# Optimization experiments

Hardware: AMD Instinct MI355X
Metric: run time of the kernel (lower is better)

## Reference

```python
import jax, jax.numpy as jnp
import numpy as np

N = 4096        # nodes
E = 4096        # hyperedges (source math forces E == N)
B = 3           # behaviors
D_IN = 64
HID = 32
OUT = 32
L = 2           # num_layers
EPS = 1e-6      # DynamicPruningGNN.epsilon
DEG_P = 0.008   # ~32 incidences per node


def setup_inputs() -> dict:
    key = jax.random.key(0)
    ks = jax.random.split(key, 12)
    sc = lambda f: 1.0 / np.sqrt(f)
    X = jax.random.normal(ks[0], (N, D_IN), jnp.float32)
    # sparse binary incidence matrices, stored dense as the original does (H.toarray())
    H = (jax.random.uniform(ks[1], (B, N, E)) < DEG_P).astype(jnp.float32)
    return {
        "X": X,
        "H": H,
        "W_init": jax.random.normal(ks[2], (D_IN, HID), jnp.float32) * sc(D_IN),
        "b_init": jnp.zeros((HID,), jnp.float32),
        "W_node": jax.random.normal(ks[3], (L, HID, HID), jnp.float32) * sc(HID),
        "b_node": jnp.zeros((L, HID), jnp.float32),
        "Theta": jax.random.normal(ks[4], (B, HID, HID), jnp.float32) * sc(HID),
        "behavior_importance": jnp.ones((B,), jnp.float32),
        "Wp1": jax.random.normal(ks[5], (HID, HID), jnp.float32) * sc(HID),
        "bp1": jnp.zeros((HID,), jnp.float32),
        "Wp2": jax.random.normal(ks[6], (HID, OUT), jnp.float32) * sc(HID),
        "bp2": jnp.zeros((OUT,), jnp.float32),
    }


def reference(X, H, W_init, b_init, W_node, b_node, Theta,
              behavior_importance, Wp1, bp1, Wp2, bp2):
    # degree normalizers, clamped like np.maximum(deg, epsilon)
    dv = 1.0 / jnp.sqrt(jnp.maximum(H.sum(axis=2), EPS))   # [B, N]  Dv^-1/2
    de = 1.0 / jnp.maximum(H.sum(axis=1), EPS)             # [B, E]  De^-1
    w = jax.nn.softmax(behavior_importance)                # behavior weights

    x = jax.nn.relu(X @ W_init + b_init)                   # initial_transform  [N, HID]
    for l in range(L):
        xw = x @ W_node[l] + b_node[l]                     # node layer          [N, HID]
        y = dv[:, :, None] * xw[None, :, :]                # Dv^-1/2 . XW       [B, N, HID]
        z = jnp.einsum('bne,bnh->beh', H, y) * de[:, :, None]   # De^-1 H^T ...  [B, E, HID]
        u = jnp.einsum('bne,beh->bnh', H, z) * dv[:, :, None]   # Dv^-1/2 H ...  [B, N, HID]
        msg = jnp.einsum('bnh,bhk->bnk', u, Theta)         # per-behavior Theta [B, N, HID]
        x = jax.nn.relu(jnp.einsum('b,bnk->nk', w, msg))   # weighted multi-behavior agg
    # node_projection: Linear -> ReLU -> Linear
    node_emb = jax.nn.relu(x @ Wp1 + bp1) @ Wp2 + bp2      # [N, OUT]
    return node_emb
```

## Files before the change

kernel.cpp:

```cpp
#include <hip/hip_runtime.h>

#define NN 4096
#define EE 4096
#define BB 3
#define DIN 64
#define HID 32
#define MAXDEG 64
#define EPSF 1e-6f
#define CCPAD 8

__global__ void build_sparse(const float* __restrict__ H,
                             int* __restrict__ rowcnt,
                             int* __restrict__ colcnt_pad,
                             unsigned short* __restrict__ csr16,
                             unsigned short* __restrict__ csc16) {
    __shared__ int el[MAXDEG];
    __shared__ int scnt;
    const int bn = blockIdx.x;
    const int tid = threadIdx.x;
    if (tid == 0) scnt = 0;
    if (tid < 32) ((unsigned int*)csc16)[bn * 32 + tid] = 0;
    if (tid < CCPAD) colcnt_pad[bn * CCPAD + tid] = 0;
    __syncthreads();
    const float4* row = (const float4*)(H + (size_t)bn * EE);
    for (int k = tid; k < EE / 4; k += 256) {
        float4 v = row[k];
        int m = (v.x != 0.f) + (v.y != 0.f) + (v.z != 0.f) + (v.w != 0.f);
        if (m) {
            int base = atomicAdd(&scnt, m);
            const int e0 = k * 4;
            if (v.x != 0.f) { if (base < MAXDEG) el[base] = e0;     base++; }
            if (v.y != 0.f) { if (base < MAXDEG) el[base] = e0 + 1; base++; }
            if (v.z != 0.f) { if (base < MAXDEG) el[base] = e0 + 2; base++; }
            if (v.w != 0.f) { if (base < MAXDEG) el[base] = e0 + 3; base++; }
        }
    }
    __syncthreads();
    const int cnt = scnt;
    if (tid == 0) rowcnt[bn] = cnt;
    const int m = min(cnt, MAXDEG);
    if (tid < MAXDEG)
        csr16[(size_t)bn * MAXDEG + tid] = (tid < m) ? (unsigned short)el[tid] : 0;
}

__global__ __launch_bounds__(256) void k_prep(
        const int* __restrict__ rowcnt, const unsigned short* __restrict__ csr16,
        int* __restrict__ colcnt_pad, unsigned short* __restrict__ csc16,
        const float* __restrict__ X,
        const float* __restrict__ Wi, const float* __restrict__ bi,
        const float* __restrict__ Wn0, const float* __restrict__ bn0,
        float* __restrict__ ybuf) {
    __shared__ float sWi[DIN * HID];
    __shared__ float sWn[HID * HID];
    __shared__ float sb0[HID], sb1[HID];
    __shared__ float su[8][HID];
    const int tid = threadIdx.x, lane = tid & 31, g = tid >> 5;
    if (blockIdx.x < NN / 8) {
        for (int i = tid; i < DIN * HID; i += 256) sWi[i] = Wi[i];
        for (int i = tid; i < HID * HID; i += 256) sWn[i] = Wn0[i];
        if (tid < HID) { sb0[tid] = bi[tid]; sb1[tid] = bn0[tid]; }
        __syncthreads();
        const int n = blockIdx.x * 8 + g;
        const float* xr = X + (size_t)n * DIN;
        float acc = sb0[lane];
#pragma unroll 8
        for (int d = 0; d < DIN; d++) acc = fmaf(xr[d], sWi[d * HID + lane], acc);
        su[g][lane] = fmaxf(acc, 0.f);
        float a = sb1[lane];
#pragma unroll
        for (int hh = 0; hh < HID; hh++) a = fmaf(su[g][hh], sWn[hh * HID + lane], a);
#pragma unroll
        for (int b = 0; b < BB; b++) {
            const float c = (float)rowcnt[(b << 12) + n];
            ybuf[((size_t)(b << 12) + n) * HID + lane] = a * rsqrtf(fmaxf(c, EPSF));
        }
    }
    const int r = blockIdx.x * 8 + g;
    const int b = r >> 12, nrel = r & (NN - 1);
    const int m = min(rowcnt[r], MAXDEG);
    const unsigned int packed = ((const unsigned int*)csr16)[r * 32 + lane];
    const int j0 = 2 * lane, j1 = 2 * lane + 1;
    if (j0 < m) {
        const int e = (int)(packed & 0xffffu);
        const int q = (b << 12) + e;
        const int slot = atomicAdd(&colcnt_pad[q * CCPAD], 1);
        if (slot < MAXDEG) csc16[(size_t)q * MAXDEG + slot] = (unsigned short)nrel;
    }
    if (j1 < m) {
        const int e = (int)(packed >> 16);
        const int q = (b << 12) + e;
        const int slot = atomicAdd(&colcnt_pad[q * CCPAD], 1);
        if (slot < MAXDEG) csc16[(size_t)q * MAXDEG + slot] = (unsigned short)nrel;
    }
}

__device__ __forceinline__ float gather16(const float* __restrict__ base,
                                          const unsigned int* __restrict__ row32,
                                          int m, int lane, int h) {
    const unsigned int packed = row32[lane];
    float a0 = 0.f, a1 = 0.f, a2 = 0.f, a3 = 0.f;
    float a4 = 0.f, a5 = 0.f, a6 = 0.f, a7 = 0.f;
    for (int j0 = 0; j0 < m; j0 += 8) {
#pragma unroll
        for (int k = 0; k < 8; k++) {
            const int j = j0 + k;
            const unsigned int p = __shfl(packed, j >> 1, 32);
            const int e = (j & 1) ? (int)(p >> 16) : (int)(p & 0xffffu);
            const float v = base[e * HID + h];
            float* acc = (k == 0) ? &a0 : (k == 1) ? &a1 : (k == 2) ? &a2 :
                         (k == 3) ? &a3 : (k == 4) ? &a4 : (k == 5) ? &a5 :
                         (k == 6) ? &a6 : &a7;
            if (j < m) *acc += v;
        }
    }
    return ((a0 + a1) + (a2 + a3)) + ((a4 + a5) + (a6 + a7));
}

__device__ __forceinline__ void softmax3(const float* __restrict__ bimp, float* sw) {
    float b0 = bimp[0], b1 = bimp[1], b2 = bimp[2];
    float m = fmaxf(b0, fmaxf(b1, b2));
    float e0 = expf(b0 - m), e1 = expf(b1 - m), e2 = expf(b2 - m);
    float s = e0 + e1 + e2;
    sw[0] = e0 / s; sw[1] = e1 / s; sw[2] = e2 / s;
}

__global__ __launch_bounds__(256) void k_z(
        const int* __restrict__ colcnt_pad, const unsigned short* __restrict__ csc16,
        const float* __restrict__ ybuf, float* __restrict__ zbuf) {
    const int tid = threadIdx.x, h = tid & 31, g = tid >> 5;
    const int q = blockIdx.x * 8 + g;
    const int cnt = colcnt_pad[q * CCPAD];
    const int m = min(cnt, MAXDEG);
    const float* yb = ybuf + (size_t)(q & ~(EE - 1)) * HID;
    const float s = gather16(yb, (const unsigned int*)csc16 + q * 32, m, h, h);
    zbuf[(size_t)q * HID + h] = s * (1.0f / fmaxf((float)cnt, EPSF));
}

__global__ __launch_bounds__(256) void k_layer(
        const float* __restrict__ zbuf,
        const int* __restrict__ rowcnt, const unsigned short* __restrict__ csr16,
        const float* __restrict__ Theta, const float* __restrict__ bimp,
        const float* __restrict__ Wn1, const float* __restrict__ bn1,
        float* __restrict__ ybuf_out) {
    __shared__ float sTh[BB * HID * HID];
    __shared__ float sW[HID * HID];
    __shared__ float sb[HID];
    __shared__ float su[8][HID];
    __shared__ float sw[4];
    const int tid = threadIdx.x;
    for (int i = tid; i < BB * HID * HID; i += 256) sTh[i] = Theta[i];
    for (int i = tid; i < HID * HID; i += 256) sW[i] = Wn1[i];
    if (tid < HID) sb[tid] = bn1[tid];
    if (tid == 0) softmax3(bimp, sw);
    __syncthreads();
    const int h = tid & 31, loc = tid >> 5;
    const int n = blockIdx.x * 8 + loc;
    float accx = 0.f;
#pragma unroll
    for (int b = 0; b < BB; b++) {
        const int r = (b << 12) + n;
        const int cnt = rowcnt[r];
        const int m = min(cnt, MAXDEG);
        const float u = gather16(zbuf + (size_t)(b << 12) * HID,
                                 (const unsigned int*)csr16 + r * 32, m, h, h)
                        * rsqrtf(fmaxf((float)cnt, EPSF));
        su[loc][h] = u;
        float msg = 0.f;
#pragma unroll
        for (int hh = 0; hh < HID; hh++)
            msg = fmaf(su[loc][hh], sTh[b * (HID * HID) + hh * HID + h], msg);
        accx = fmaf(sw[b], msg, accx);
    }
    su[loc][h] = fmaxf(accx, 0.f);
    float a = sb[h];
#pragma unroll
    for (int hh = 0; hh < HID; hh++) a = fmaf(su[loc][hh], sW[hh * HID + h], a);
#pragma unroll
    for (int b = 0; b < BB; b++) {
        const float c = (float)rowcnt[(b << 12) + n];
        ybuf_out[((size_t)(b << 12) + n) * HID + h] = a * rsqrtf(fmaxf(c, EPSF));
    }
}

__global__ __launch_bounds__(256) void k_final(
        const float* __restrict__ zbuf,
        const int* __restrict__ rowcnt, const unsigned short* __restrict__ csr16,
        const float* __restrict__ Theta, const float* __restrict__ bimp,
        const float* __restrict__ Wp1, const float* __restrict__ bp1,
        const float* __restrict__ Wp2, const float* __restrict__ bp2,
        float* __restrict__ out) {
    __shared__ float sTh[BB * HID * HID];
    __shared__ float sW1[HID * HID], sW2[HID * HID];
    __shared__ float sb1[HID], sb2[HID];
    __shared__ float su[8][HID];
    __shared__ float sw[4];
    const int tid = threadIdx.x;
    for (int i = tid; i < BB * HID * HID; i += 256) sTh[i] = Theta[i];
    for (int i = tid; i < HID * HID; i += 256) { sW1[i] = Wp1[i]; sW2[i] = Wp2[i]; }
    if (tid < HID) { sb1[tid] = bp1[tid]; sb2[tid] = bp2[tid]; }
    if (tid == 0) softmax3(bimp, sw);
    __syncthreads();
    const int h = tid & 31, loc = tid >> 5;
    const int n = blockIdx.x * 8 + loc;
    float accx = 0.f;
#pragma unroll
    for (int b = 0; b < BB; b++) {
        const int r = (b << 12) + n;
        const int cnt = rowcnt[r];
        const int m = min(cnt, MAXDEG);
        const float u = gather16(zbuf + (size_t)(b << 12) * HID,
                                 (const unsigned int*)csr16 + r * 32, m, h, h)
                        * rsqrtf(fmaxf((float)cnt, EPSF));
        su[loc][h] = u;
        float msg = 0.f;
#pragma unroll
        for (int hh = 0; hh < HID; hh++)
            msg = fmaf(su[loc][hh], sTh[b * (HID * HID) + hh * HID + h], msg);
        accx = fmaf(sw[b], msg, accx);
    }
    su[loc][h] = fmaxf(accx, 0.f);
    float p = sb1[h];
#pragma unroll
    for (int hh = 0; hh < HID; hh++) p = fmaf(su[loc][hh], sW1[hh * HID + h], p);
    su[loc][h] = fmaxf(p, 0.f);
    float o = sb2[h];
#pragma unroll
    for (int hh = 0; hh < HID; hh++) o = fmaf(su[loc][hh], sW2[hh * HID + h], o);
    out[(size_t)n * HID + h] = o;
}

extern "C" void kernel_launch(void* const* d_in, const int* in_sizes, int n_in,
                              void* d_out, int out_size, void* d_ws, size_t ws_size,
                              hipStream_t stream) {
    const float* X      = (const float*)d_in[0];
    const float* H      = (const float*)d_in[1];
    const float* W_init = (const float*)d_in[2];
    const float* b_init = (const float*)d_in[3];
    const float* W_node = (const float*)d_in[4];
    const float* b_node = (const float*)d_in[5];
    const float* Theta  = (const float*)d_in[6];
    const float* bimp   = (const float*)d_in[7];
    const float* Wp1    = (const float*)d_in[8];
    const float* bp1    = (const float*)d_in[9];
    const float* Wp2    = (const float*)d_in[10];
    const float* bp2    = (const float*)d_in[11];
    float* out = (float*)d_out;
    (void)in_sizes; (void)n_in; (void)out_size; (void)ws_size;

    char* ws = (char*)d_ws;
    size_t off = 0;
    auto alloc = [&](size_t bytes) { void* p = ws + off; off += (bytes + 255) & ~(size_t)255; return p; };
    int*            rowcnt     = (int*)alloc((size_t)BB * NN * 4);
    int*            colcnt_pad = (int*)alloc((size_t)BB * EE * CCPAD * 4);
    unsigned short* csr16      = (unsigned short*)alloc((size_t)BB * NN * MAXDEG * 2);
    unsigned short* csc16      = (unsigned short*)alloc((size_t)BB * EE * MAXDEG * 2);
    float*          ybuf       = (float*)alloc((size_t)BB * NN * HID * 4);
    float*          zbuf       = (float*)alloc((size_t)BB * EE * HID * 4);

    build_sparse<<<BB * NN, 256, 0, stream>>>(H, rowcnt, colcnt_pad, csr16, csc16);
    k_prep<<<(BB * NN) / 8, 256, 0, stream>>>(rowcnt, csr16, colcnt_pad, csc16,
                                              X, W_init, b_init, W_node, b_node, ybuf);
    k_z<<<(BB * EE) / 8, 256, 0, stream>>>(colcnt_pad, csc16, ybuf, zbuf);
    k_layer<<<NN / 8, 256, 0, stream>>>(zbuf, rowcnt, csr16, Theta, bimp,
                                        W_node + HID * HID, b_node + HID, ybuf);
    k_z<<<(BB * EE) / 8, 256, 0, stream>>>(colcnt_pad, csc16, ybuf, zbuf);
    k_final<<<NN / 8, 256, 0, stream>>>(zbuf, rowcnt, csr16, Theta, bimp,
                                        Wp1, bp1, Wp2, bp2, out);
}
```

Before: 362.7 us.

## Fuse sparse build, CSC scatter and initial transform into one kernel

Merges the incidence scan, the CSC scatter and the initial node transform into a single build kernel, with a tiny zeroing kernel for the column counts. Node features are now stored once per node instead of once per behavior, and Dv^-1/2 is applied inside the z gather from a precomputed dvinv array. This cuts the launch count and drops the replicated y buffer writes. In exchange the z gather does an extra indexed load per neighbor, and the column counts lose their padding, so atomic contention may rise. Gather loops are also restructured to issue all eight loads before accumulating.

```diff
diff --git a/kernel.cpp b/kernel.cpp
--- a/kernel.cpp
+++ b/kernel.cpp
@@ -7,27 +7,33 @@
 #define HID 32
 #define MAXDEG 64
 #define EPSF 1e-6f
-#define CCPAD 8
-
-__global__ void build_sparse(const float* __restrict__ H,
-                             int* __restrict__ rowcnt,
-                             int* __restrict__ colcnt_pad,
-                             unsigned short* __restrict__ csr16,
-                             unsigned short* __restrict__ csc16) {
+
+__global__ void k_zero(int* __restrict__ p, int n) {
+    const int i = blockIdx.x * 256 + threadIdx.x;
+    if (i < n) p[i] = 0;
+}
+
+__global__ __launch_bounds__(256) void build_all(
+        const float* __restrict__ H, const float* __restrict__ X,
+        const float* __restrict__ Wi, const float* __restrict__ bi,
+        const float* __restrict__ Wn0, const float* __restrict__ bn0,
+        int* __restrict__ rowcnt, float* __restrict__ dvinv,
+        int* __restrict__ colcnt,
+        unsigned short* __restrict__ csr16, unsigned short* __restrict__ csc16,
+        float* __restrict__ xw0) {
     __shared__ int el[MAXDEG];
     __shared__ int scnt;
-    const int bn = blockIdx.x;
-    const int tid = threadIdx.x;
+    __shared__ float sh[HID];
+    const int bn = blockIdx.x, tid = threadIdx.x;
+    const int b = bn >> 12, nrel = bn & (NN - 1);
     if (tid == 0) scnt = 0;
-    if (tid < 32) ((unsigned int*)csc16)[bn * 32 + tid] = 0;
-    if (tid < CCPAD) colcnt_pad[bn * CCPAD + tid] = 0;
     __syncthreads();
     const float4* row = (const float4*)(H + (size_t)bn * EE);
     for (int k = tid; k < EE / 4; k += 256) {
         float4 v = row[k];
-        int m = (v.x != 0.f) + (v.y != 0.f) + (v.z != 0.f) + (v.w != 0.f);
-        if (m) {
-            int base = atomicAdd(&scnt, m);
+        int mm = (v.x != 0.f) + (v.y != 0.f) + (v.z != 0.f) + (v.w != 0.f);
+        if (mm) {
+            int base = atomicAdd(&scnt, mm);
             const int e0 = k * 4;
             if (v.x != 0.f) { if (base < MAXDEG) el[base] = e0;     base++; }
             if (v.y != 0.f) { if (base < MAXDEG) el[base] = e0 + 1; base++; }
@@ -37,103 +43,85 @@
     }
     __syncthreads();
     const int cnt = scnt;
-    if (tid == 0) rowcnt[bn] = cnt;
     const int m = min(cnt, MAXDEG);
+    if (tid == 0) {
+        rowcnt[bn] = cnt;
+        dvinv[bn] = rsqrtf(fmaxf((float)cnt, EPSF));
+    }
     if (tid < MAXDEG)
         csr16[(size_t)bn * MAXDEG + tid] = (tid < m) ? (unsigned short)el[tid] : 0;
-}
-
-__global__ __launch_bounds__(256) void k_prep(
-        const int* __restrict__ rowcnt, const unsigned short* __restrict__ csr16,
-        int* __restrict__ colcnt_pad, unsigned short* __restrict__ csc16,
-        const float* __restrict__ X,
-        const float* __restrict__ Wi, const float* __restrict__ bi,
-        const float* __restrict__ Wn0, const float* __restrict__ bn0,
-        float* __restrict__ ybuf) {
-    __shared__ float sWi[DIN * HID];
-    __shared__ float sWn[HID * HID];
-    __shared__ float sb0[HID], sb1[HID];
-    __shared__ float su[8][HID];
-    const int tid = threadIdx.x, lane = tid & 31, g = tid >> 5;
-    if (blockIdx.x < NN / 8) {
-        for (int i = tid; i < DIN * HID; i += 256) sWi[i] = Wi[i];
-        for (int i = tid; i < HID * HID; i += 256) sWn[i] = Wn0[i];
-        if (tid < HID) { sb0[tid] = bi[tid]; sb1[tid] = bn0[tid]; }
-        __syncthreads();
-        const int n = blockIdx.x * 8 + g;
-        const float* xr = X + (size_t)n * DIN;
-        float acc = sb0[lane];
+    if (tid < m) {
+        const int q = (b << 12) + el[tid];
+        const int slot = atomicAdd(&colcnt[q], 1);
+        if (slot < MAXDEG) csc16[(size_t)q * MAXDEG + slot] = (unsigned short)nrel;
+    }
+    if (b == 0 && tid < HID) {
+        const int h = tid;
+        const float* xr = X + (size_t)nrel * DIN;
+        float acc = bi[h];
 #pragma unroll 8
-        for (int d = 0; d < DIN; d++) acc = fmaf(xr[d], sWi[d * HID + lane], acc);
-        su[g][lane] = fmaxf(acc, 0.f);
-        float a = sb1[lane];
-#pragma unroll
-        for (int hh = 0; hh < HID; hh++) a = fmaf(su[g][hh], sWn[hh * HID + lane], a);
-#pragma unroll
-        for (int b = 0; b < BB; b++) {
-            const float c = (float)rowcnt[(b << 12) + n];
-            ybuf[((size_t)(b << 12) + n) * HID + lane] = a * rsqrtf(fmaxf(c, EPSF));
-        }
-    }
-    const int r = blockIdx.x * 8 + g;
-    const int b = r >> 12, nrel = r & (NN - 1);
-    const int m = min(rowcnt[r], MAXDEG);
-    const unsigned int packed = ((const unsigned int*)csr16)[r * 32 + lane];
-    const int j0 = 2 * lane, j1 = 2 * lane + 1;
-    if (j0 < m) {
-        const int e = (int)(packed & 0xffffu);
-        const int q = (b << 12) + e;
-        const int slot = atomicAdd(&colcnt_pad[q * CCPAD], 1);
-        if (slot < MAXDEG) csc16[(size_t)q * MAXDEG + slot] = (unsigned short)nrel;
-    }
-    if (j1 < m) {
-        const int e = (int)(packed >> 16);
-        const int q = (b << 12) + e;
-        const int slot = atomicAdd(&colcnt_pad[q * CCPAD], 1);
-        if (slot < MAXDEG) csc16[(size_t)q * MAXDEG + slot] = (unsigned short)nrel;
-    }
-}
-
-__device__ __forceinline__ float gather16(const float* __restrict__ base,
-                                          const unsigned int* __restrict__ row32,
-                                          int m, int lane, int h) {
-    const unsigned int packed = row32[lane];
-    float a0 = 0.f, a1 = 0.f, a2 = 0.f, a3 = 0.f;
-    float a4 = 0.f, a5 = 0.f, a6 = 0.f, a7 = 0.f;
+        for (int d = 0; d < DIN; d++) acc = fmaf(xr[d], Wi[d * HID + h], acc);
+        sh[h] = fmaxf(acc, 0.f);
+        float a = bn0[h];
+#pragma unroll
+        for (int k = 0; k < HID; k++) a = fmaf(sh[k], Wn0[k * HID + h], a);
+        xw0[nrel * HID + h] = a;
+    }
+}
+
+__global__ __launch_bounds__(256) void k_z(
+        const int* __restrict__ colcnt, const unsigned short* __restrict__ csc16,
+        const float* __restrict__ xw, const float* __restrict__ dvinv,
+        float* __restrict__ zbuf) {
+    const int tid = threadIdx.x, h = tid & 31, g = tid >> 5;
+    const int q = blockIdx.x * 8 + g;
+    const int cnt = colcnt[q];
+    const int m = min(cnt, MAXDEG);
+    const int dvbase = q & ~(NN - 1);
+    const unsigned int packed = ((const unsigned int*)csc16)[q * 32 + h];
+    float acc[8] = {0.f, 0.f, 0.f, 0.f, 0.f, 0.f, 0.f, 0.f};
     for (int j0 = 0; j0 < m; j0 += 8) {
+        float vs[8];
 #pragma unroll
         for (int k = 0; k < 8; k++) {
             const int j = j0 + k;
             const unsigned int p = __shfl(packed, j >> 1, 32);
-            const int e = (j & 1) ? (int)(p >> 16) : (int)(p & 0xffffu);
-            const float v = base[e * HID + h];
-            float* acc = (k == 0) ? &a0 : (k == 1) ? &a1 : (k == 2) ? &a2 :
-                         (k == 3) ? &a3 : (k == 4) ? &a4 : (k == 5) ? &a5 :
-                         (k == 6) ? &a6 : &a7;
-            if (j < m) *acc += v;
+            const int id = (j & 1) ? (int)(p >> 16) : (int)(p & 0xffffu);
+            vs[k] = xw[id * HID + h] * dvinv[dvbase + id];
         }
-    }
-    return ((a0 + a1) + (a2 + a3)) + ((a4 + a5) + (a6 + a7));
+#pragma unroll
+        for (int k = 0; k < 8; k++) if (j0 + k < m) acc[k] += vs[k];
+    }
+    const float s = ((acc[0] + acc[1]) + (acc[2] + acc[3]))
+                  + ((acc[4] + acc[5]) + (acc[6] + acc[7]));
+    zbuf[(size_t)q * HID + h] = s * (1.0f / fmaxf((float)cnt, EPSF));
+}
+
+__device__ __forceinline__ float gatherz(const float* __restrict__ zb,
+                                         unsigned int packed, int m, int h) {
+    float acc[8] = {0.f, 0.f, 0.f, 0.f, 0.f, 0.f, 0.f, 0.f};
+    for (int j0 = 0; j0 < m; j0 += 8) {
+        float vs[8];
+#pragma unroll
+        for (int k = 0; k < 8; k++) {
+            const int j = j0 + k;
+            const unsigned int p = __shfl(packed, j >> 1, 32);
+            const int id = (j & 1) ? (int)(p >> 16) : (int)(p & 0xffffu);
+            vs[k] = zb[id * HID + h];
+        }
+#pragma unroll
+        for (int k = 0; k < 8; k++) if (j0 + k < m) acc[k] += vs[k];
+    }
+    return ((acc[0] + acc[1]) + (acc[2] + acc[3]))
+         + ((acc[4] + acc[5]) + (acc[6] + acc[7]));
 }
 
 __device__ __forceinline__ void softmax3(const float* __restrict__ bimp, float* sw) {
     float b0 = bimp[0], b1 = bimp[1], b2 = bimp[2];
-    float m = fmaxf(b0, fmaxf(b1, b2));
-    float e0 = expf(b0 - m), e1 = expf(b1 - m), e2 = expf(b2 - m);
+    float mm = fmaxf(b0, fmaxf(b1, b2));
+    float e0 = expf(b0 - mm), e1 = expf(b1 - mm), e2 = expf(b2 - mm);
     float s = e0 + e1 + e2;
     sw[0] = e0 / s; sw[1] = e1 / s; sw[2] = e2 / s;
-}
-
-__global__ __launch_bounds__(256) void k_z(
-        const int* __restrict__ colcnt_pad, const unsigned short* __restrict__ csc16,
-        const float* __restrict__ ybuf, float* __restrict__ zbuf) {
-    const int tid = threadIdx.x, h = tid & 31, g = tid >> 5;
-    const int q = blockIdx.x * 8 + g;
-    const int cnt = colcnt_pad[q * CCPAD];
-    const int m = min(cnt, MAXDEG);
-    const float* yb = ybuf + (size_t)(q & ~(EE - 1)) * HID;
-    const float s = gather16(yb, (const unsigned int*)csc16 + q * 32, m, h, h);
-    zbuf[(size_t)q * HID + h] = s * (1.0f / fmaxf((float)cnt, EPSF));
 }
 
 __global__ __launch_bounds__(256) void k_layer(
@@ -141,7 +129,7 @@
         const int* __restrict__ rowcnt, const unsigned short* __restrict__ csr16,
         const float* __restrict__ Theta, const float* __restrict__ bimp,
         const float* __restrict__ Wn1, const float* __restrict__ bn1,
-        float* __restrict__ ybuf_out) {
+        float* __restrict__ xw1) {
     __shared__ float sTh[BB * HID * HID];
     __shared__ float sW[HID * HID];
     __shared__ float sb[HID];
@@ -161,8 +149,8 @@
         const int r = (b << 12) + n;
         const int cnt = rowcnt[r];
         const int m = min(cnt, MAXDEG);
-        const float u = gather16(zbuf + (size_t)(b << 12) * HID,
-                                 (const unsigned int*)csr16 + r * 32, m, h, h)
+        const unsigned int packed = ((const unsigned int*)csr16)[r * 32 + h];
+        const float u = gatherz(zbuf + (size_t)(b << 12) * HID, packed, m, h)
                         * rsqrtf(fmaxf((float)cnt, EPSF));
         su[loc][h] = u;
         float msg = 0.f;
@@ -175,11 +163,7 @@
     float a = sb[h];
 #pragma unroll
     for (int hh = 0; hh < HID; hh++) a = fmaf(su[loc][hh], sW[hh * HID + h], a);
-#pragma unroll
-    for (int b = 0; b < BB; b++) {
-        const float c = (float)rowcnt[(b << 12) + n];
-        ybuf_out[((size_t)(b << 12) + n) * HID + h] = a * rsqrtf(fmaxf(c, EPSF));
-    }
+    xw1[n * HID + h] = a;
 }
 
 __global__ __launch_bounds__(256) void k_final(
@@ -208,8 +192,8 @@
         const int r = (b << 12) + n;
         const int cnt = rowcnt[r];
         const int m = min(cnt, MAXDEG);
-        const float u = gather16(zbuf + (size_t)(b << 12) * HID,
-                                 (const unsigned int*)csr16 + r * 32, m, h, h)
+        const unsigned int packed = ((const unsigned int*)csr16)[r * 32 + h];
+        const float u = gatherz(zbuf + (size_t)(b << 12) * HID, packed, m, h)
                         * rsqrtf(fmaxf((float)cnt, EPSF));
         su[loc][h] = u;
         float msg = 0.f;
@@ -250,20 +234,22 @@
     char* ws = (char*)d_ws;
     size_t off = 0;
     auto alloc = [&](size_t bytes) { void* p = ws + off; off += (bytes + 255) & ~(size_t)255; return p; };
-    int*            rowcnt     = (int*)alloc((size_t)BB * NN * 4);
-    int*            colcnt_pad = (int*)alloc((size_t)BB * EE * CCPAD * 4);
-    unsigned short* csr16      = (unsigned short*)alloc((size_t)BB * NN * MAXDEG * 2);
-    unsigned short* csc16      = (unsigned short*)alloc((size_t)BB * EE * MAXDEG * 2);
-    float*          ybuf       = (float*)alloc((size_t)BB * NN * HID * 4);
-    float*          zbuf       = (float*)alloc((size_t)BB * EE * HID * 4);
-
-    build_sparse<<<BB * NN, 256, 0, stream>>>(H, rowcnt, colcnt_pad, csr16, csc16);
-    k_prep<<<(BB * NN) / 8, 256, 0, stream>>>(rowcnt, csr16, colcnt_pad, csc16,
-                                              X, W_init, b_init, W_node, b_node, ybuf);
-    k_z<<<(BB * EE) / 8, 256, 0, stream>>>(colcnt_pad, csc16, ybuf, zbuf);
+    int*            rowcnt = (int*)alloc((size_t)BB * NN * 4);
+    float*          dvinv  = (float*)alloc((size_t)BB * NN * 4);
+    int*            colcnt = (int*)alloc((size_t)BB * EE * 4);
+    unsigned short* csr16  = (unsigned short*)alloc((size_t)BB * NN * MAXDEG * 2);
+    unsigned short* csc16  = (unsigned short*)alloc((size_t)BB * EE * MAXDEG * 2);
+    float*          xw0    = (float*)alloc((size_t)NN * HID * 4);
+    float*          xw1    = (float*)alloc((size_t)NN * HID * 4);
+    float*          zbuf   = (float*)alloc((size_t)BB * EE * HID * 4);
+
+    k_zero<<<(BB * EE + 255) / 256, 256, 0, stream>>>(colcnt, BB * EE);
+    build_all<<<BB * NN, 256, 0, stream>>>(H, X, W_init, b_init, W_node, b_node,
+                                           rowcnt, dvinv, colcnt, csr16, csc16, xw0);
+    k_z<<<(BB * EE) / 8, 256, 0, stream>>>(colcnt, csc16, xw0, dvinv, zbuf);
     k_layer<<<NN / 8, 256, 0, stream>>>(zbuf, rowcnt, csr16, Theta, bimp,
-                                        W_node + HID * HID, b_node + HID, ybuf);
-    k_z<<<(BB * EE) / 8, 256, 0, stream>>>(colcnt_pad, csc16, ybuf, zbuf);
+                                        W_node + HID * HID, b_node + HID, xw1);
+    k_z<<<(BB * EE) / 8, 256, 0, stream>>>(colcnt, csc16, xw1, dvinv, zbuf);
     k_final<<<NN / 8, 256, 0, stream>>>(zbuf, rowcnt, csr16, Theta, bimp,
                                         Wp1, bp1, Wp2, bp2, out);
 }
```

New measurement: 344.3 us. -5.1%, faster.
